# Kernel tuning notes

Hardware: AMD Instinct MI355X
Metric: run time of the kernel (lower is better)

Reference implementation:

```python
import jax, jax.numpy as jnp
import numpy as np

N_HEADS = 16


def setup_inputs() -> dict:
    key = jax.random.key(0)
    k1, k2, k3 = jax.random.split(key, 3)
    dim = 1024
    # ragged batch: 16 sequences with lengths 64..1024 (step 64), total_nnz = 8704
    lengths = np.arange(64, 1025, 64, dtype=np.int32)  # (16,)
    cu_seqlens = jnp.asarray(np.concatenate([[0], np.cumsum(lengths)]), dtype=jnp.int32)  # (17,)
    total_nnz = int(lengths.sum())  # 8704
    max_seqlen = int(lengths.max())  # 1024
    hidden_states = jax.random.normal(k1, (total_nnz, dim), dtype=jnp.float32)
    # nn.Linear(dim, 3*dim): weight (3*dim, dim), bias (3*dim)
    Wqkv_weight = jax.random.normal(k2, (3 * dim, dim), dtype=jnp.float32) * (dim ** -0.5)
    Wqkv_bias = jax.random.normal(k3, (3 * dim,), dtype=jnp.float32) * 0.02
    return {
        "hidden_states": hidden_states,
        "Wqkv_weight": Wqkv_weight,
        "Wqkv_bias": Wqkv_bias,
        "cu_seqlens": cu_seqlens,
        "max_seqlen": max_seqlen,
    }


def reference(hidden_states, Wqkv_weight, Wqkv_bias, cu_seqlens, max_seqlen):
    # Unpadded (varlen) self-attention, p_dropout = 0 (eval path).
    nnz, dim = hidden_states.shape
    H = N_HEADS
    D = dim // H
    S = int(max_seqlen)  # static pad length
    B = cu_seqlens.shape[0] - 1

    qkv = hidden_states @ Wqkv_weight.T + Wqkv_bias          # (nnz, 3*dim)
    qkv = qkv.reshape(nnz, 3, H, D)

    seqlens = cu_seqlens[1:] - cu_seqlens[:-1]                # (B,)
    pos = jnp.arange(S)
    valid = pos[None, :] < seqlens[:, None]                   # (B, S) token validity
    gather_idx = jnp.where(valid, cu_seqlens[:-1, None] + pos[None, :], 0)

    qkv_pad = qkv[gather_idx]                                 # (B, S, 3, H, D)
    q = qkv_pad[:, :, 0]                                      # (B, S, H, D)
    k = qkv_pad[:, :, 1]
    v = qkv_pad[:, :, 2]

    scale = 1.0 / jnp.sqrt(jnp.asarray(D, dtype=q.dtype))
    scores = jnp.einsum("bshd,bthd->bhst", q, k) * scale      # (B, H, S, S)
    neg_inf = jnp.asarray(-1e9, dtype=scores.dtype)
    scores = jnp.where(valid[:, None, None, :], scores, neg_inf)  # mask invalid keys
    attn = jax.nn.softmax(scores, axis=-1)
    out_pad = jnp.einsum("bhst,bthd->bshd", attn, v)          # (B, S, H, D)

    # scatter back to unpadded layout (nnz, H*D)
    tok = jnp.arange(nnz)
    tok_b = jnp.searchsorted(cu_seqlens, tok, side="right") - 1
    tok_s = tok - cu_seqlens[tok_b]
    out = out_pad[tok_b, tok_s].reshape(nnz, H * D)
    return out
```

## Files before the change

### kernel.cpp

```cpp
#include <hip/hip_runtime.h>
#include <math.h>


#define HD 64

typedef _Float16 half8 __attribute__((ext_vector_type(8)));
typedef _Float16 half4v __attribute__((ext_vector_type(4)));
typedef float f32x4 __attribute__((ext_vector_type(4)));

#define GLP(p) ((__attribute__((address_space(1))) void*)(p))
#define LDSP(p) ((__attribute__((address_space(3))) void*)(p))

__global__ __launch_bounds__(256)
void cvt_kernel(const float* __restrict__ A, const float* __restrict__ W,
                _Float16* __restrict__ Ah, _Float16* __restrict__ Wh,
                int nA4, int nW4)
{
    int total = nA4 + nW4;
    for (int i = blockIdx.x * blockDim.x + threadIdx.x; i < total;
         i += gridDim.x * blockDim.x) {
        const float* src; _Float16* dst; int j;
        if (i < nA4) { src = A; dst = Ah; j = i; }
        else         { src = W; dst = Wh; j = i - nA4; }
        float4 v = *(const float4*)(src + (size_t)j * 4);
        half4v h;
        h.x = (_Float16)v.x; h.y = (_Float16)v.y;
        h.z = (_Float16)v.z; h.w = (_Float16)v.w;
        *(half4v*)(dst + (size_t)j * 4) = h;
    }
}

__global__ __launch_bounds__(256)
void qkv_gemm_kernel(const _Float16* __restrict__ Ah, const _Float16* __restrict__ Wh,
                     const float* __restrict__ bias,
                     _Float16* __restrict__ Qo, _Float16* __restrict__ Ko,
                     _Float16* __restrict__ Vo,
                     int Kd, int dim)
{
    const int bm = blockIdx.x, bn = blockIdx.y;
    const int t = threadIdx.x;
    const int wid = t >> 6, lane = t & 63;
    const int wr = wid >> 1, wc = wid & 1;
    const int fr = lane & 15, fq = lane >> 4;

    __shared__ _Float16 As[128 * 32];
    __shared__ _Float16 Bs[128 * 32];

    const int m0 = bm * 128, n0 = bn * 128;

    f32x4 acc[4][4];
#pragma unroll
    for (int m = 0; m < 4; ++m)
#pragma unroll
        for (int n = 0; n < 4; ++n) acc[m][n] = (f32x4)0.f;

    float biasv[4];
#pragma unroll
    for (int n = 0; n < 4; ++n)
        biasv[n] = bias[n0 + wc * 64 + n * 16 + fr];

    const int c0 = t, c1 = t + 256;

    for (int k0 = 0; k0 < Kd; k0 += 32) {
        __syncthreads();
        {
            const _Float16* Ab = Ah + (size_t)m0 * Kd + k0;
            const _Float16* Bb = Wh + (size_t)n0 * Kd + k0;
            __builtin_amdgcn_global_load_lds(GLP(Ab + (c0 >> 2) * Kd + (c0 & 3) * 8),
                                             LDSP((char*)As + c0 * 16), 16, 0, 0);
            __builtin_amdgcn_global_load_lds(GLP(Ab + (c1 >> 2) * Kd + (c1 & 3) * 8),
                                             LDSP((char*)As + c1 * 16), 16, 0, 0);
            __builtin_amdgcn_global_load_lds(GLP(Bb + (c0 >> 2) * Kd + (c0 & 3) * 8),
                                             LDSP((char*)Bs + c0 * 16), 16, 0, 0);
            __builtin_amdgcn_global_load_lds(GLP(Bb + (c1 >> 2) * Kd + (c1 & 3) * 8),
                                             LDSP((char*)Bs + c1 * 16), 16, 0, 0);
        }
        __syncthreads();

        half8 a[4], b[4];
#pragma unroll
        for (int m = 0; m < 4; ++m)
            a[m] = *(const half8*)&As[(wr * 64 + m * 16 + fr) * 32 + fq * 8];
#pragma unroll
        for (int n = 0; n < 4; ++n)
            b[n] = *(const half8*)&Bs[(wc * 64 + n * 16 + fr) * 32 + fq * 8];
#pragma unroll
        for (int m = 0; m < 4; ++m)
#pragma unroll
            for (int n = 0; n < 4; ++n)
                acc[m][n] = __builtin_amdgcn_mfma_f32_16x16x32_f16(a[m], b[n], acc[m][n], 0, 0, 0);
    }

    const int which = n0 / dim;
    const int offb  = n0 - which * dim;
    _Float16* dst = (which == 0) ? Qo : (which == 1) ? Ko : Vo;
#pragma unroll
    for (int m = 0; m < 4; ++m) {
#pragma unroll
        for (int n = 0; n < 4; ++n) {
            int gc = offb + wc * 64 + n * 16 + fr;
#pragma unroll
            for (int j = 0; j < 4; ++j) {
                int gm = m0 + wr * 64 + m * 16 + fq * 4 + j;
                dst[(size_t)gm * dim + gc] = (_Float16)(acc[m][n][j] + biasv[n]);
            }
        }
    }
}

__global__ __launch_bounds__(256)
void attn_kernel(const _Float16* __restrict__ Q, const _Float16* __restrict__ K,
                 const _Float16* __restrict__ V, const int* __restrict__ cu,
                 float* __restrict__ out, int dim, int H, int B)
{
    const int w  = blockIdx.x;
    const int h  = w & (H - 1);
    const int wq = w / H;

    int b = -1, qt = 0, acc = 0;
    for (int i = B - 1; i >= 0; --i) {
        int Li = cu[i + 1] - cu[i];
        int nq = (Li + 127) >> 7;
        if (wq >= acc && wq < acc + nq) { b = i; qt = wq - acc; }
        acc += nq;
    }
    if (b < 0) return;

    const int s0 = cu[b];
    const int L  = cu[b + 1] - s0;

    const int t    = threadIdx.x;
    const int wid  = t >> 6, lane = t & 63;
    const int fr   = lane & 15, fq = lane >> 4;

    __shared__ _Float16 Ks[64 * 64];
    __shared__ _Float16 Vt[64 * 72];
    __shared__ _Float16 Ps[4][32 * 72];
    __shared__ float    Fs[4][32];

    _Float16* Psw = &Ps[wid][0];
    float*    Fsw = &Fs[wid][0];

    const _Float16 qscale = (_Float16)(0.125f * 1.44269504f);
    half8 aq[2][2];
#pragma unroll
    for (int nt = 0; nt < 2; ++nt)
#pragma unroll
        for (int kc = 0; kc < 2; ++kc) {
            int qrow = qt * 128 + wid * 32 + nt * 16 + fr;
            int qr = (qrow < L) ? qrow : 0;
            half8 v = *(const half8*)(Q + (size_t)(s0 + qr) * dim + h * HD + kc * 32 + fq * 8);
#pragma unroll
            for (int i = 0; i < 8; ++i) v[i] = v[i] * qscale;
            aq[nt][kc] = v;
        }

    f32x4 o[2][4];
    float m2[2], l2[2];
#pragma unroll
    for (int qm = 0; qm < 2; ++qm)
#pragma unroll
        for (int n = 0; n < 4; ++n) o[qm][n] = (f32x4)0.f;
    m2[0] = m2[1] = -3.0e38f;
    l2[0] = l2[1] = 0.f;

    const int nkt = (L + 63) >> 6;
    const int vu = t & 31, vdc = t >> 5;

    for (int kt = 0; kt < nkt; ++kt) {
        __syncthreads();

#pragma unroll
        for (int cc = 0; cc < 2; ++cc) {
            int c    = wid * 2 + cc;
            int phys = c * 1024 + lane * 16;
            int r    = phys >> 7;
            int lb   = (phys & 127) ^ ((r & 7) << 4);
            int krow = kt * 64 + r;
            int kr   = (krow < L) ? krow : 0;
            const char* src = (const char*)K + ((size_t)(s0 + kr) * dim + h * HD) * 2 + lb;
            __builtin_amdgcn_global_load_lds(GLP(src), LDSP((char*)Ks + phys), 16, 0, 0);
        }
        {
            int k0r = kt * 64 + vu * 2;
            int r0 = (k0r     < L) ? k0r     : 0;
            int r1 = (k0r + 1 < L) ? k0r + 1 : 0;
            half8 v0 = *(const half8*)(V + (size_t)(s0 + r0) * dim + h * HD + vdc * 8);
            half8 v1 = *(const half8*)(V + (size_t)(s0 + r1) * dim + h * HD + vdc * 8);
#pragma unroll
            for (int i = 0; i < 8; ++i) {
                union { _Float16 h[2]; unsigned u; } pk;
                pk.h[0] = v0[i]; pk.h[1] = v1[i];
                *(unsigned*)&Vt[(vdc * 8 + i) * 72 + vu * 2] = pk.u;
            }
        }
        __syncthreads();

        f32x4 s2[4][2];
#pragma unroll
        for (int mt = 0; mt < 4; ++mt)
#pragma unroll
            for (int nt = 0; nt < 2; ++nt) s2[mt][nt] = (f32x4)0.f;

#pragma unroll
        for (int mt = 0; mt < 4; ++mt)
#pragma unroll
            for (int kc = 0; kc < 2; ++kc) {
                const half8 bk = *(const half8*)((const char*)Ks +
                    ((mt * 16 + fr) << 7) + (((kc << 6) + (fq << 4)) ^ ((fr & 7) << 4)));
                s2[mt][0] = __builtin_amdgcn_mfma_f32_16x16x32_f16(bk, aq[0][kc], s2[mt][0], 0, 0, 0);
                s2[mt][1] = __builtin_amdgcn_mfma_f32_16x16x32_f16(bk, aq[1][kc], s2[mt][1], 0, 0, 0);
            }

        int ksz = L - kt * 64;
        if (ksz < 64) {
#pragma unroll
            for (int mt = 0; mt < 4; ++mt)
#pragma unroll
                for (int j = 0; j < 4; ++j)
                    if (mt * 16 + fq * 4 + j >= ksz) {
                        s2[mt][0][j] = -1.0e30f;
                        s2[mt][1][j] = -1.0e30f;
                    }
        }

#pragma unroll
        for (int nt = 0; nt < 2; ++nt) {
            f32x4 mx4 = s2[0][nt];
#pragma unroll
            for (int mt = 1; mt < 4; ++mt) {
#pragma unroll
                for (int j = 0; j < 4; ++j) mx4[j] = fmaxf(mx4[j], s2[mt][nt][j]);
            }
            float mx = fmaxf(fmaxf(mx4[0], mx4[1]), fmaxf(mx4[2], mx4[3]));
            mx = fmaxf(mx, __shfl_xor(mx, 16));
            mx = fmaxf(mx, __shfl_xor(mx, 32));
            float mnew = fmaxf(m2[nt], mx);
            float facn = __builtin_exp2f(m2[nt] - mnew);
            m2[nt] = mnew;

            f32x4 sum4 = (f32x4)0.f;
#pragma unroll
            for (int mt = 0; mt < 4; ++mt) {
                half4v ph;
#pragma unroll
                for (int j = 0; j < 4; ++j) {
                    float p = __builtin_exp2f(s2[mt][nt][j] - mnew);
                    sum4[j] += p;
                    ph[j] = (_Float16)p;
                }
                *(half4v*)&Psw[(nt * 16 + fr) * 72 + mt * 16 + fq * 4] = ph;
            }
            float ls = (sum4[0] + sum4[1]) + (sum4[2] + sum4[3]);
            ls += __shfl_xor(ls, 16);
            ls += __shfl_xor(ls, 32);
            l2[nt] = l2[nt] * facn + ls;
            if (fq == 0) Fsw[nt * 16 + fr] = facn;
        }

#pragma unroll
        for (int qm = 0; qm < 2; ++qm) {
            f32x4 fj = *(const f32x4*)&Fsw[qm * 16 + fq * 4];
#pragma unroll
            for (int n2 = 0; n2 < 4; ++n2)
#pragma unroll
                for (int j = 0; j < 4; ++j) o[qm][n2][j] *= fj[j];
        }

#pragma unroll
        for (int kc = 0; kc < 2; ++kc) {
            half8 ap0 = *(const half8*)&Psw[(0 * 16 + fr) * 72 + kc * 32 + fq * 8];
            half8 ap1 = *(const half8*)&Psw[(1 * 16 + fr) * 72 + kc * 32 + fq * 8];
#pragma unroll
            for (int n2 = 0; n2 < 4; ++n2) {
                half8 bv = *(const half8*)&Vt[(n2 * 16 + fr) * 72 + kc * 32 + fq * 8];
                o[0][n2] = __builtin_amdgcn_mfma_f32_16x16x32_f16(ap0, bv, o[0][n2], 0, 0, 0);
                o[1][n2] = __builtin_amdgcn_mfma_f32_16x16x32_f16(ap1, bv, o[1][n2], 0, 0, 0);
            }
        }
    }

    if (fq == 0) { Fsw[fr] = l2[0]; Fsw[16 + fr] = l2[1]; }
#pragma unroll
    for (int qm = 0; qm < 2; ++qm) {
        f32x4 lj = *(const f32x4*)&Fsw[qm * 16 + fq * 4];
#pragma unroll
        for (int j = 0; j < 4; ++j) {
            int qrow = qt * 128 + wid * 32 + qm * 16 + fq * 4 + j;
            if (qrow >= L) continue;
            float inv = 1.0f / lj[j];
#pragma unroll
            for (int n2 = 0; n2 < 4; ++n2)
                out[(size_t)(s0 + qrow) * dim + h * HD + n2 * 16 + fr] = o[qm][n2][j] * inv;
        }
    }
}

extern "C" void kernel_launch(void* const* d_in, const int* in_sizes, int n_in,
                              void* d_out, int out_size, void* d_ws, size_t ws_size,
                              hipStream_t stream)
{
    const float* hs   = (const float*)d_in[0];
    const float* W    = (const float*)d_in[1];
    const float* bias = (const float*)d_in[2];
    const int*   cu   = (const int*)d_in[3];

    const int dim3x = in_sizes[2];
    const int dim   = dim3x / 3;
    const int nnz   = in_sizes[0] / dim;
    const int B     = in_sizes[3] - 1;
    const int H     = dim / HD;
    const size_t nA = (size_t)nnz * dim;
    const size_t nW = (size_t)dim3x * dim;

    _Float16* Ah = (_Float16*)d_ws;
    _Float16* Wh = Ah + nA;
    _Float16* Qh = Wh + nW;
    _Float16* Kh = Qh + nA;
    _Float16* Vh = Kh + nA;

    cvt_kernel<<<1024, 256, 0, stream>>>(hs, W, Ah, Wh, (int)(nA / 4), (int)(nW / 4));

    dim3 g1(nnz / 128, dim3x / 128);
    qkv_gemm_kernel<<<g1, 256, 0, stream>>>(Ah, Wh, bias, Qh, Kh, Vh, dim, dim);

    const int maxWQ = nnz / 128 + B;
    attn_kernel<<<maxWQ * H, 256, 0, stream>>>(Qh, Kh, Vh, cu, (float*)d_out, dim, H, B);
}
```

Measured before the change: 259.6 us.

## Double GEMM K-tile to 64 and XOR-swizzle LDS layout to avoid bank conflicts

The QKV GEMM now loads a K-depth of 64 per iteration instead of 32, which halves the number of barrier pairs and global-to-LDS rounds. It also applies an XOR swizzle on 16-byte chunks, done through the global source address so the LDS destination stays linear, to remove LDS bank conflicts on the half8 fragment reads. LDS use per block doubles to 32 KB, which may lower occupancy.

Result: faster. 244.3 us (-5.9%).

```diff
diff --git a/kernel.cpp b/kernel.cpp
--- a/kernel.cpp
+++ b/kernel.cpp
@@ -43,8 +43,8 @@
     const int wr = wid >> 1, wc = wid & 1;
     const int fr = lane & 15, fq = lane >> 4;
 
-    __shared__ _Float16 As[128 * 32];
-    __shared__ _Float16 Bs[128 * 32];
+    __shared__ _Float16 As[128 * 64];
+    __shared__ _Float16 Bs[128 * 64];
 
     const int m0 = bm * 128, n0 = bn * 128;
 
@@ -59,36 +59,51 @@
     for (int n = 0; n < 4; ++n)
         biasv[n] = bias[n0 + wc * 64 + n * 16 + fr];
 
-    const int c0 = t, c1 = t + 256;
-
-    for (int k0 = 0; k0 < Kd; k0 += 32) {
+    int srow[4], slb[4];
+#pragma unroll
+    for (int i = 0; i < 4; ++i) {
+        int c = t + 256 * i;
+        srow[i] = c >> 3;
+        slb[i]  = ((c & 7) << 4) ^ ((srow[i] & 7) << 4);
+    }
+
+    for (int k0 = 0; k0 < Kd; k0 += 64) {
         __syncthreads();
         {
-            const _Float16* Ab = Ah + (size_t)m0 * Kd + k0;
-            const _Float16* Bb = Wh + (size_t)n0 * Kd + k0;
-            __builtin_amdgcn_global_load_lds(GLP(Ab + (c0 >> 2) * Kd + (c0 & 3) * 8),
-                                             LDSP((char*)As + c0 * 16), 16, 0, 0);
-            __builtin_amdgcn_global_load_lds(GLP(Ab + (c1 >> 2) * Kd + (c1 & 3) * 8),
-                                             LDSP((char*)As + c1 * 16), 16, 0, 0);
-            __builtin_amdgcn_global_load_lds(GLP(Bb + (c0 >> 2) * Kd + (c0 & 3) * 8),
-                                             LDSP((char*)Bs + c0 * 16), 16, 0, 0);
-            __builtin_amdgcn_global_load_lds(GLP(Bb + (c1 >> 2) * Kd + (c1 & 3) * 8),
-                                             LDSP((char*)Bs + c1 * 16), 16, 0, 0);
+            const char* Ab = (const char*)Ah + ((size_t)m0 * Kd + k0) * 2;
+            const char* Bb = (const char*)Wh + ((size_t)n0 * Kd + k0) * 2;
+#pragma unroll
+            for (int i = 0; i < 4; ++i) {
+                int phys = (t + 256 * i) * 16;
+                __builtin_amdgcn_global_load_lds(GLP(Ab + (size_t)srow[i] * Kd * 2 + slb[i]),
+                                                 LDSP((char*)As + phys), 16, 0, 0);
+                __builtin_amdgcn_global_load_lds(GLP(Bb + (size_t)srow[i] * Kd * 2 + slb[i]),
+                                                 LDSP((char*)Bs + phys), 16, 0, 0);
+            }
         }
         __syncthreads();
 
-        half8 a[4], b[4];
-#pragma unroll
-        for (int m = 0; m < 4; ++m)
-            a[m] = *(const half8*)&As[(wr * 64 + m * 16 + fr) * 32 + fq * 8];
-#pragma unroll
-        for (int n = 0; n < 4; ++n)
-            b[n] = *(const half8*)&Bs[(wc * 64 + n * 16 + fr) * 32 + fq * 8];
-#pragma unroll
-        for (int m = 0; m < 4; ++m)
-#pragma unroll
-            for (int n = 0; n < 4; ++n)
-                acc[m][n] = __builtin_amdgcn_mfma_f32_16x16x32_f16(a[m], b[n], acc[m][n], 0, 0, 0);
+#pragma unroll
+        for (int kc = 0; kc < 2; ++kc) {
+            half8 a[4], b[4];
+#pragma unroll
+            for (int m = 0; m < 4; ++m) {
+                int row = wr * 64 + m * 16 + fr;
+                a[m] = *(const half8*)((const char*)As + row * 128 +
+                        ((kc * 64 + fq * 16) ^ ((fr & 7) << 4)));
+            }
+#pragma unroll
+            for (int n = 0; n < 4; ++n) {
+                int row = wc * 64 + n * 16 + fr;
+                b[n] = *(const half8*)((const char*)Bs + row * 128 +
+                        ((kc * 64 + fq * 16) ^ ((fr & 7) << 4)));
+            }
+#pragma unroll
+            for (int m = 0; m < 4; ++m)
+#pragma unroll
+                for (int n = 0; n < 4; ++n)
+                    acc[m][n] = __builtin_amdgcn_mfma_f32_16x16x32_f16(a[m], b[n], acc[m][n], 0, 0, 0);
+        }
     }
 
     const int which = n0 / dim;
```
